# Performance work log

Hardware: AMD Instinct MI355X
Metric: run time of the kernel (lower is better)

Reference implementation:

```python
import jax, jax.numpy as jnp
import numpy as np

L1, L2, L3, L4 = 0.01, 0.001, 0.1, 100.0
DROP_P = 0.3

def setup_inputs() -> dict:
    key = jax.random.key(0)
    ks = jax.random.split(key, 6)
    n, p, h, c = 262144, 256, 256, 10
    x = jax.random.normal(ks[0], (n, p), dtype=jnp.float32)
    y = jax.random.randint(ks[1], (n,), 0, c, dtype=jnp.int64)
    drop_u = jax.random.uniform(ks[2], (n, h), dtype=jnp.float32)
    b1 = jax.random.normal(ks[3], (p, h), dtype=jnp.float32) / p
    b2 = jax.random.normal(ks[4], (h, c), dtype=jnp.float32) / h
    w = jax.random.normal(ks[5], (n, 1), dtype=jnp.float32) / n + 1.0 / np.sqrt(n).astype(np.float32)
    return {"x": x, "y": y, "drop_u": drop_u, "b1": b1, "b2": b2, "w": w}

def reference(x, y, drop_u, b1, b2, w):
    n, p = x.shape
    # MLP: ReLU -> Dropout(0.3) (inverted dropout, deterministic mask from drop_u)
    hdn = jax.nn.relu(x @ b1)
    keep = (drop_u > DROP_P).astype(x.dtype) / (1.0 - DROP_P)
    logits = (hdn * keep) @ b2  # [n, 10]
    pred = jnp.argmax(logits, axis=1)
    weight = w * w  # [n, 1]
    # per-sample CE; torch broadcast ce[n] * weight[n,1] -> [n,n], summed == ce.sum()*weight.sum()
    ce = -jnp.take_along_axis(jax.nn.log_softmax(logits, axis=-1), y[:, None], axis=1)[:, 0]
    loss = ce.sum() * weight.sum()
    # balancing regularizer: x.T @ diag(weight) @ x computed as column-scale-then-GEMM
    col = x.T @ weight  # [p, 1]
    gram = x.T @ (weight * x)  # [p, p] == x.T @ diag(weight) @ x
    bm = (gram - col @ col.T) * (1.0 - jnp.eye(p, dtype=x.dtype))
    loss = loss + L1 * (jnp.abs(b1).sum() + jnp.abs(b2).sum())
    loss = loss + L2 * jnp.sum(bm * bm)
    loss = loss + L3 * jnp.sum(weight * weight)
    loss = loss + L4 * (weight.sum() - 1.0) ** 2
    acc = jnp.mean((pred == y).astype(jnp.float32))
    return (loss, acc)
```

## Files before the change

### kernel.cpp

```cpp
#include <hip/hip_runtime.h>
#include <hip/hip_bf16.h>
#include <math.h>

typedef __bf16 v8bf  __attribute__((ext_vector_type(8)));
typedef __bf16 v4bf  __attribute__((ext_vector_type(4)));
typedef float  v16f  __attribute__((ext_vector_type(16)));
typedef float  v4f   __attribute__((ext_vector_type(4)));
typedef float  f4v   __attribute__((ext_vector_type(4)));

#define OFF_COL   16
#define OFF_WT    512
#define OFF_SLOT  262656
#define B1T_BYTE  68159488
#define B2T_BYTE  68290560
#define ZERO_BYTES 1088

extern "C" __global__ __launch_bounds__(256) void prep_k(
    const float* __restrict__ w, const float* __restrict__ b1,
    const float* __restrict__ b2, float* __restrict__ wsf) {
  float* weight = wsf + OFF_WT;
  __bf16* b1T = (__bf16*)((char*)wsf + B1T_BYTE);
  __bf16* b2T = (__bf16*)((char*)wsf + B2T_BYTE);
  int gid = blockIdx.x * 256 + threadIdx.x;
  float wi = w[gid];
  float wt = wi * wi;
  weight[gid] = wt;
  float s1 = wt, s2 = wt * wt, a1 = 0.f, a2 = 0.f;
  if (gid < 65536) {
    int h = gid >> 8, p = gid & 255;
    float v = b1[p * 256 + h];
    b1T[gid] = (__bf16)v;
    a1 = fabsf(v);
  }
  if (gid < 4096) {
    int c = gid >> 8, h = gid & 255;
    float v = (c < 10) ? b2[h * 10 + c] : 0.f;
    b2T[gid] = (__bf16)v;
    a2 = fabsf(v);
  }
  #pragma unroll
  for (int off = 32; off > 0; off >>= 1) {
    s1 += __shfl_down(s1, off);
    s2 += __shfl_down(s2, off);
    a1 += __shfl_down(a1, off);
    a2 += __shfl_down(a2, off);
  }
  if ((threadIdx.x & 63) == 0) {
    atomicAdd(&wsf[1], s1);
    atomicAdd(&wsf[2], s2);
    if (blockIdx.x < 256) atomicAdd(&wsf[3], a1);
    if (blockIdx.x < 16)  atomicAdd(&wsf[4], a2);
  }
}

extern "C" __global__ __launch_bounds__(512, 2) void gram_k(
    const float* __restrict__ x, float* __restrict__ wsf) {
  const float* weight = wsf + OFF_WT;
  float* slot = wsf + OFF_SLOT + blockIdx.x * 65536;
  __shared__ __bf16 xT[2][256 * 72];
  __shared__ __bf16 wxT[2][256 * 72];
  __shared__ float  wS[1024];
  const int tid = threadIdx.x;
  const int wv = tid >> 6, L = tid & 63;
  const int l32 = L & 31, lh = L >> 5;
  const int mb = 64 * (wv >> 1), nb = 128 * (wv & 1);
  const int col = tid & 255, rh = tid >> 8;
  const int base = blockIdx.x * 1024;
  v16f acc[2][4] = {};
  float colAcc = 0.f;
  float xv[32];

  wS[tid] = weight[base + tid];
  wS[tid + 512] = weight[base + 512 + tid];

  #pragma unroll
  for (int j = 0; j < 32; j++)
    xv[j] = x[(base + 32 * rh + j) * 256 + col];
  __syncthreads();
  #pragma unroll
  for (int s = 0; s < 8; s++) {
    v4bf xa, wa;
    #pragma unroll
    for (int i = 0; i < 4; i++) {
      int kr = 32 * rh + 4 * s + i;
      float v = xv[4 * s + i];
      float wvv = wS[kr] * v;
      colAcc += wvv;
      xa[i] = (__bf16)v;
      wa[i] = (__bf16)wvv;
    }
    *(v4bf*)&xT[0][col * 72 + 32 * rh + 4 * s]  = xa;
    *(v4bf*)&wxT[0][col * 72 + 32 * rh + 4 * s] = wa;
  }
  __syncthreads();

  for (int ch = 0; ch < 16; ch++) {
    const int cur = ch & 1, nxt = cur ^ 1;
    if (ch < 15) {
      int k0 = base + 64 * (ch + 1);
      #pragma unroll
      for (int j = 0; j < 32; j++)
        xv[j] = x[(k0 + 32 * rh + j) * 256 + col];
    }
    #pragma unroll
    for (int ks = 0; ks < 64; ks += 16) {
      v8bf a0 = *(const v8bf*)&xT[cur][(mb + l32) * 72 + ks + 8 * lh];
      v8bf a1 = *(const v8bf*)&xT[cur][(mb + 32 + l32) * 72 + ks + 8 * lh];
      v8bf b[4];
      #pragma unroll
      for (int tn = 0; tn < 4; tn++)
        b[tn] = *(const v8bf*)&wxT[cur][(nb + 32 * tn + l32) * 72 + ks + 8 * lh];
      #pragma unroll
      for (int tn = 0; tn < 4; tn++) {
        acc[0][tn] = __builtin_amdgcn_mfma_f32_32x32x16_bf16(a0, b[tn], acc[0][tn], 0, 0, 0);
        acc[1][tn] = __builtin_amdgcn_mfma_f32_32x32x16_bf16(a1, b[tn], acc[1][tn], 0, 0, 0);
      }
    }
    if (ch < 15) {
      const int wb = 64 * (ch + 1);
      #pragma unroll
      for (int s = 0; s < 8; s++) {
        v4bf xa, wa;
        #pragma unroll
        for (int i = 0; i < 4; i++) {
          int kr = 32 * rh + 4 * s + i;
          float v = xv[4 * s + i];
          float wvv = wS[wb + kr] * v;
          colAcc += wvv;
          xa[i] = (__bf16)v;
          wa[i] = (__bf16)wvv;
        }
        *(v4bf*)&xT[nxt][col * 72 + 32 * rh + 4 * s]  = xa;
        *(v4bf*)&wxT[nxt][col * 72 + 32 * rh + 4 * s] = wa;
      }
      __syncthreads();
    }
  }

  #pragma unroll
  for (int tm = 0; tm < 2; tm++)
    #pragma unroll
    for (int tn = 0; tn < 4; tn++)
      #pragma unroll
      for (int r = 0; r < 16; r++) {
        int row = mb + 32 * tm + (r & 3) + 8 * (r >> 2) + 4 * lh;
        int cg = nb + 32 * tn + l32;
        slot[row * 256 + cg] = acc[tm][tn][r];
      }
  atomicAdd(&wsf[OFF_COL + col], colAcc);
}

extern "C" __global__ __launch_bounds__(256) void gfin_k(float* __restrict__ wsf) {
  __shared__ float partial[4][256];
  const int tid = threadIdx.x;
  const int sg = tid >> 6, l = tid & 63;
  const int row = blockIdx.x;
  const float* slot0 = wsf + OFF_SLOT;
  f4v s = {0.f, 0.f, 0.f, 0.f};
  #pragma unroll 4
  for (int sl = sg; sl < 256; sl += 4)
    s += ((const f4v*)(slot0 + sl * 65536 + row * 256))[l];
  *(f4v*)&partial[sg][4 * l] = s;
  __syncthreads();
  float cr = wsf[OFF_COL + row];
  float ct = wsf[OFF_COL + tid];
  float gv = partial[0][tid] + partial[1][tid] + partial[2][tid] + partial[3][tid];
  float d = gv - cr * ct;
  float bm = (tid != row) ? d * d : 0.f;
  #pragma unroll
  for (int off = 32; off > 0; off >>= 1) bm += __shfl_down(bm, off);
  if (l == 0) atomicAdd(&wsf[5], bm);
}

extern "C" __global__ __launch_bounds__(256, 4) void mlp_k(
    const float* __restrict__ x, const int* __restrict__ y,
    const float* __restrict__ du, float* __restrict__ wsf) {
  const __bf16* b1T = (const __bf16*)((const char*)wsf + B1T_BYTE);
  const __bf16* b2T = (const __bf16*)((const char*)wsf + B2T_BYTE);
  __shared__ union U {
    struct { __bf16 xs[64 * 40]; __bf16 b1s[256 * 40]; } m;
    struct { __bf16 hk[64 * 264]; float lg[64 * 16]; } l;
  } sm;
  const int tid = threadIdx.x;
  const int wv = tid >> 6, L = tid & 63;
  const int l32 = L & 31, lh = L >> 5;
  const int nb = 64 * wv;
  const int rowBase = blockIdx.x * 64;

  v16f acc[2][2] = {};

  for (int kc = 0; kc < 256; kc += 32) {
    __syncthreads();
    #pragma unroll
    for (int i = 0; i < 2; i++) {
      int f = tid + 256 * i;
      int r = f >> 3, c4 = f & 7;
      f4v v = ((const f4v*)x)[(rowBase + r) * 64 + (kc >> 2) + c4];
      v4bf o;
      o[0] = (__bf16)v[0]; o[1] = (__bf16)v[1]; o[2] = (__bf16)v[2]; o[3] = (__bf16)v[3];
      *(v4bf*)&sm.m.xs[r * 40 + 4 * c4] = o;
    }
    #pragma unroll
    for (int i = 0; i < 4; i++) {
      int f = tid + 256 * i;
      int nr = f >> 2, c = f & 3;
      *(v8bf*)&sm.m.b1s[nr * 40 + 8 * c] = *(const v8bf*)&b1T[nr * 256 + kc + 8 * c];
    }
    __syncthreads();
    #pragma unroll
    for (int ks = 0; ks < 32; ks += 16) {
      v8bf a0 = *(const v8bf*)&sm.m.xs[(l32) * 40 + ks + 8 * lh];
      v8bf a1 = *(const v8bf*)&sm.m.xs[(32 + l32) * 40 + ks + 8 * lh];
      v8bf b0 = *(const v8bf*)&sm.m.b1s[(nb + l32) * 40 + ks + 8 * lh];
      v8bf b1f = *(const v8bf*)&sm.m.b1s[(nb + 32 + l32) * 40 + ks + 8 * lh];
      acc[0][0] = __builtin_amdgcn_mfma_f32_32x32x16_bf16(a0, b0,  acc[0][0], 0, 0, 0);
      acc[0][1] = __builtin_amdgcn_mfma_f32_32x32x16_bf16(a0, b1f, acc[0][1], 0, 0, 0);
      acc[1][0] = __builtin_amdgcn_mfma_f32_32x32x16_bf16(a1, b0,  acc[1][0], 0, 0, 0);
      acc[1][1] = __builtin_amdgcn_mfma_f32_32x32x16_bf16(a1, b1f, acc[1][1], 0, 0, 0);
    }
  }
  #pragma unroll
  for (int tm = 0; tm < 2; tm++)
    #pragma unroll
    for (int tn = 0; tn < 2; tn++)
      #pragma unroll
      for (int r = 0; r < 16; r++) {
        int row = 32 * tm + (r & 3) + 8 * (r >> 2) + 4 * lh;
        int cg = nb + 32 * tn + l32;
        float u = du[(rowBase + row) * 256 + cg];
        float v = acc[tm][tn][r];
        v = fmaxf(v, 0.f);
        acc[tm][tn][r] = (u > 0.3f) ? v * (1.0f / 0.7f) : 0.f;
      }

  __syncthreads();
  #pragma unroll
  for (int tm = 0; tm < 2; tm++)
    #pragma unroll
    for (int tn = 0; tn < 2; tn++)
      #pragma unroll
      for (int r = 0; r < 16; r++) {
        int row = 32 * tm + (r & 3) + 8 * (r >> 2) + 4 * lh;
        int cg = nb + 32 * tn + l32;
        sm.l.hk[row * 264 + cg] = (__bf16)acc[tm][tn][r];
      }
  __syncthreads();
  v4f lacc = {};
  #pragma unroll
  for (int kk = 0; kk < 8; kk++) {
    v8bf a  = *(const v8bf*)&sm.l.hk[(16 * wv + (L & 15)) * 264 + 32 * kk + 8 * (L >> 4)];
    v8bf bb = *(const v8bf*)&b2T[(L & 15) * 256 + 32 * kk + 8 * (L >> 4)];
    lacc = __builtin_amdgcn_mfma_f32_16x16x32_bf16(a, bb, lacc, 0, 0, 0);
  }
  #pragma unroll
  for (int r = 0; r < 4; r++)
    sm.l.lg[(16 * wv + 4 * (L >> 4) + r) * 16 + (L & 15)] = lacc[r];
  __syncthreads();
  float ce = 0.f;
  int cor = 0;
  if (tid < 64) {
    const float* lr = &sm.l.lg[tid * 16];
    float mx = lr[0];
    int am = 0;
    #pragma unroll
    for (int c = 1; c < 10; c++)
      if (lr[c] > mx) { mx = lr[c]; am = c; }
    float s = 0.f;
    #pragma unroll
    for (int c = 0; c < 10; c++) s += expf(lr[c] - mx);
    int yt = y[rowBase + tid];
    ce = logf(s) + mx - lr[yt];
    cor = (am == yt) ? 1 : 0;
  }
  if (wv == 0) {
    #pragma unroll
    for (int off = 32; off > 0; off >>= 1) ce += __shfl_down(ce, off);
    unsigned long long bal = __ballot(cor != 0);
    if (L == 0) {
      atomicAdd(&wsf[0], ce);
      atomicAdd((int*)&wsf[8], (int)__popcll(bal));
    }
  }
}

extern "C" __global__ void fin2_k(const float* __restrict__ wsf, float* __restrict__ out) {
  if (threadIdx.x == 0) {
    float ce = wsf[0], wsum = wsf[1], w4 = wsf[2], ab1 = wsf[3], ab2 = wsf[4], bm = wsf[5];
    int cor = ((const int*)wsf)[8];
    float loss = ce * wsum
               + 0.01f * (ab1 + ab2)
               + 0.001f * bm
               + 0.1f * w4
               + 100.f * (wsum - 1.f) * (wsum - 1.f);
    out[0] = loss;
    out[1] = (float)cor * (1.0f / 262144.0f);
  }
}

extern "C" void kernel_launch(void* const* d_in, const int* in_sizes, int n_in,
                              void* d_out, int out_size, void* d_ws, size_t ws_size,
                              hipStream_t stream) {
  const float* x  = (const float*)d_in[0];
  const int*   y  = (const int*)d_in[1];
  const float* du = (const float*)d_in[2];
  const float* b1 = (const float*)d_in[3];
  const float* b2 = (const float*)d_in[4];
  const float* w  = (const float*)d_in[5];
  float* wsf = (float*)d_ws;

  hipMemsetAsync(d_ws, 0, ZERO_BYTES, stream);
  prep_k<<<1024, 256, 0, stream>>>(w, b1, b2, wsf);
  gram_k<<<256, 512, 0, stream>>>(x, wsf);
  gfin_k<<<256, 256, 0, stream>>>(wsf);
  mlp_k<<<4096, 256, 0, stream>>>(x, y, du, wsf);
  fin2_k<<<1, 64, 0, stream>>>(wsf, (float*)d_out);
}
```

Measured before the change: 769.2 us.

## Register-prefetch next K-chunk of x/b1 and early-load dropout mask in mlp_k

The GEMM main loop now loads the next 32-wide K chunk of x and b1T into registers while MFMAs run on the current chunk in shared memory, which overlaps global latency with compute. Half of the dropout uniforms are loaded into registers during the second-to-last chunk so their latency is hidden before the epilogue. The logits scratch row stride is padded from 16 to 17 floats to avoid LDS bank conflicts. In exchange it adds register pressure (prefetch vectors plus 32 floats of dropout values) under a launch-bounds occupancy target of 4.

```diff
diff --git a/kernel.cpp b/kernel.cpp
--- a/kernel.cpp
+++ b/kernel.cpp
@@ -179,7 +179,7 @@
   const __bf16* b2T = (const __bf16*)((const char*)wsf + B2T_BYTE);
   __shared__ union U {
     struct { __bf16 xs[64 * 40]; __bf16 b1s[256 * 40]; } m;
-    struct { __bf16 hk[64 * 264]; float lg[64 * 16]; } l;
+    struct { __bf16 hk[64 * 264]; float lg[64 * 17]; } l;
   } sm;
   const int tid = threadIdx.x;
   const int wv = tid >> 6, L = tid & 63;
@@ -187,31 +187,62 @@
   const int nb = 64 * wv;
   const int rowBase = blockIdx.x * 64;
 
+  const int xr = tid >> 3, xc = tid & 7;
+  const int bnr = tid >> 2, bc = tid & 3;
+
   v16f acc[2][2] = {};
-
-  for (int kc = 0; kc < 256; kc += 32) {
+  f4v  xp0, xp1;
+  v8bf bp0, bp1, bp2, bp3;
+  float dup[32];
+
+  {
+    const int kc = 0;
+    xp0 = ((const f4v*)x)[(rowBase + xr) * 64 + (kc >> 2) + xc];
+    xp1 = ((const f4v*)x)[(rowBase + 32 + xr) * 64 + (kc >> 2) + xc];
+    bp0 = *(const v8bf*)&b1T[(bnr      ) * 256 + kc + 8 * bc];
+    bp1 = *(const v8bf*)&b1T[(bnr +  64) * 256 + kc + 8 * bc];
+    bp2 = *(const v8bf*)&b1T[(bnr + 128) * 256 + kc + 8 * bc];
+    bp3 = *(const v8bf*)&b1T[(bnr + 192) * 256 + kc + 8 * bc];
+  }
+
+  #pragma unroll
+  for (int ch = 0; ch < 8; ch++) {
     __syncthreads();
-    #pragma unroll
-    for (int i = 0; i < 2; i++) {
-      int f = tid + 256 * i;
-      int r = f >> 3, c4 = f & 7;
-      f4v v = ((const f4v*)x)[(rowBase + r) * 64 + (kc >> 2) + c4];
+    {
       v4bf o;
-      o[0] = (__bf16)v[0]; o[1] = (__bf16)v[1]; o[2] = (__bf16)v[2]; o[3] = (__bf16)v[3];
-      *(v4bf*)&sm.m.xs[r * 40 + 4 * c4] = o;
-    }
-    #pragma unroll
-    for (int i = 0; i < 4; i++) {
-      int f = tid + 256 * i;
-      int nr = f >> 2, c = f & 3;
-      *(v8bf*)&sm.m.b1s[nr * 40 + 8 * c] = *(const v8bf*)&b1T[nr * 256 + kc + 8 * c];
+      o[0] = (__bf16)xp0[0]; o[1] = (__bf16)xp0[1]; o[2] = (__bf16)xp0[2]; o[3] = (__bf16)xp0[3];
+      *(v4bf*)&sm.m.xs[xr * 40 + 4 * xc] = o;
+      o[0] = (__bf16)xp1[0]; o[1] = (__bf16)xp1[1]; o[2] = (__bf16)xp1[2]; o[3] = (__bf16)xp1[3];
+      *(v4bf*)&sm.m.xs[(xr + 32) * 40 + 4 * xc] = o;
+      *(v8bf*)&sm.m.b1s[(bnr      ) * 40 + 8 * bc] = bp0;
+      *(v8bf*)&sm.m.b1s[(bnr +  64) * 40 + 8 * bc] = bp1;
+      *(v8bf*)&sm.m.b1s[(bnr + 128) * 40 + 8 * bc] = bp2;
+      *(v8bf*)&sm.m.b1s[(bnr + 192) * 40 + 8 * bc] = bp3;
     }
     __syncthreads();
+    if (ch < 7) {
+      const int kc = 32 * (ch + 1);
+      xp0 = ((const f4v*)x)[(rowBase + xr) * 64 + (kc >> 2) + xc];
+      xp1 = ((const f4v*)x)[(rowBase + 32 + xr) * 64 + (kc >> 2) + xc];
+      bp0 = *(const v8bf*)&b1T[(bnr      ) * 256 + kc + 8 * bc];
+      bp1 = *(const v8bf*)&b1T[(bnr +  64) * 256 + kc + 8 * bc];
+      bp2 = *(const v8bf*)&b1T[(bnr + 128) * 256 + kc + 8 * bc];
+      bp3 = *(const v8bf*)&b1T[(bnr + 192) * 256 + kc + 8 * bc];
+    }
+    if (ch == 6) {
+      #pragma unroll
+      for (int tn = 0; tn < 2; tn++)
+        #pragma unroll
+        for (int r = 0; r < 16; r++) {
+          int row = (r & 3) + 8 * (r >> 2) + 4 * lh;
+          dup[tn * 16 + r] = du[(rowBase + row) * 256 + nb + 32 * tn + l32];
+        }
+    }
     #pragma unroll
     for (int ks = 0; ks < 32; ks += 16) {
-      v8bf a0 = *(const v8bf*)&sm.m.xs[(l32) * 40 + ks + 8 * lh];
-      v8bf a1 = *(const v8bf*)&sm.m.xs[(32 + l32) * 40 + ks + 8 * lh];
-      v8bf b0 = *(const v8bf*)&sm.m.b1s[(nb + l32) * 40 + ks + 8 * lh];
+      v8bf a0  = *(const v8bf*)&sm.m.xs[(l32) * 40 + ks + 8 * lh];
+      v8bf a1  = *(const v8bf*)&sm.m.xs[(32 + l32) * 40 + ks + 8 * lh];
+      v8bf b0  = *(const v8bf*)&sm.m.b1s[(nb + l32) * 40 + ks + 8 * lh];
       v8bf b1f = *(const v8bf*)&sm.m.b1s[(nb + 32 + l32) * 40 + ks + 8 * lh];
       acc[0][0] = __builtin_amdgcn_mfma_f32_32x32x16_bf16(a0, b0,  acc[0][0], 0, 0, 0);
       acc[0][1] = __builtin_amdgcn_mfma_f32_32x32x16_bf16(a0, b1f, acc[0][1], 0, 0, 0);
@@ -220,18 +251,22 @@
     }
   }
   #pragma unroll
-  for (int tm = 0; tm < 2; tm++)
-    #pragma unroll
-    for (int tn = 0; tn < 2; tn++)
-      #pragma unroll
-      for (int r = 0; r < 16; r++) {
-        int row = 32 * tm + (r & 3) + 8 * (r >> 2) + 4 * lh;
-        int cg = nb + 32 * tn + l32;
-        float u = du[(rowBase + row) * 256 + cg];
-        float v = acc[tm][tn][r];
-        v = fmaxf(v, 0.f);
-        acc[tm][tn][r] = (u > 0.3f) ? v * (1.0f / 0.7f) : 0.f;
-      }
+  for (int tn = 0; tn < 2; tn++)
+    #pragma unroll
+    for (int r = 0; r < 16; r++) {
+      float u = dup[tn * 16 + r];
+      float v = fmaxf(acc[0][tn][r], 0.f);
+      acc[0][tn][r] = (u > 0.3f) ? v * (1.0f / 0.7f) : 0.f;
+    }
+  #pragma unroll
+  for (int tn = 0; tn < 2; tn++)
+    #pragma unroll
+    for (int r = 0; r < 16; r++) {
+      int row = 32 + (r & 3) + 8 * (r >> 2) + 4 * lh;
+      float u = du[(rowBase + row) * 256 + nb + 32 * tn + l32];
+      float v = fmaxf(acc[1][tn][r], 0.f);
+      acc[1][tn][r] = (u > 0.3f) ? v * (1.0f / 0.7f) : 0.f;
+    }
 
   __syncthreads();
   #pragma unroll
@@ -254,12 +289,12 @@
   }
   #pragma unroll
   for (int r = 0; r < 4; r++)
-    sm.l.lg[(16 * wv + 4 * (L >> 4) + r) * 16 + (L & 15)] = lacc[r];
+    sm.l.lg[(16 * wv + 4 * (L >> 4) + r) * 17 + (L & 15)] = lacc[r];
   __syncthreads();
   float ce = 0.f;
   int cor = 0;
   if (tid < 64) {
-    const float* lr = &sm.l.lg[tid * 16];
+    const float* lr = &sm.l.lg[tid * 17];
     float mx = lr[0];
     int am = 0;
     #pragma unroll
```

Result: slower. 807.8 us (+5.0%).

## Prefetch dropout uniforms during GEMM loop and pack into shared bitmask

Applied to the files above, without the earlier changes.

The dropout uniforms used to be read with scattered scalar global loads after the first GEMM. They are now streamed as coalesced float4 loads spread across the k-chunk loop, using a small register ring that hides load latency behind the MFMA work. Each load is converted into a 4-bit keep mask in shared memory, and the epilogue reads that mask instead of global memory. The logits staging array is also padded to stride 17 to cut LDS bank conflicts. In exchange the kernel holds 24 more live float registers, which could reduce occupancy at 4 waves per SIMD, and it uses 4 KB more LDS in the GEMM phase.

```diff
diff --git a/kernel.cpp b/kernel.cpp
--- a/kernel.cpp
+++ b/kernel.cpp
@@ -178,18 +178,22 @@
   const __bf16* b1T = (const __bf16*)((const char*)wsf + B1T_BYTE);
   const __bf16* b2T = (const __bf16*)((const char*)wsf + B2T_BYTE);
   __shared__ union U {
-    struct { __bf16 xs[64 * 40]; __bf16 b1s[256 * 40]; } m;
-    struct { __bf16 hk[64 * 264]; float lg[64 * 16]; } l;
+    struct { __bf16 xs[64 * 40]; __bf16 b1s[256 * 40]; unsigned char msk[4096]; } m;
+    struct { __bf16 hk[64 * 264]; float lg[64 * 17]; } l;
   } sm;
   const int tid = threadIdx.x;
   const int wv = tid >> 6, L = tid & 63;
   const int l32 = L & 31, lh = L >> 5;
   const int nb = 64 * wv;
   const int rowBase = blockIdx.x * 64;
+  const f4v* du4 = (const f4v*)du + (size_t)rowBase * 64;
 
   v16f acc[2][2] = {};
-
-  for (int kc = 0; kc < 256; kc += 32) {
+  f4v dq[6];
+
+  #pragma unroll
+  for (int ch = 0; ch < 8; ch++) {
+    const int kc = 32 * ch;
     __syncthreads();
     #pragma unroll
     for (int i = 0; i < 2; i++) {
@@ -207,11 +211,24 @@
       *(v8bf*)&sm.m.b1s[nr * 40 + 8 * c] = *(const v8bf*)&b1T[nr * 256 + kc + 8 * c];
     }
     __syncthreads();
+    dq[(2 * ch) % 6]     = du4[tid + 256 * (2 * ch)];
+    dq[(2 * ch + 1) % 6] = du4[tid + 256 * (2 * ch + 1)];
+    if (ch >= 2) {
+      const int i0 = 2 * ch - 4, i1 = 2 * ch - 3;
+      f4v d0 = dq[i0 % 6];
+      sm.m.msk[tid + 256 * i0] = (unsigned char)(
+          (d0[0] > 0.3f ? 1 : 0) | (d0[1] > 0.3f ? 2 : 0) |
+          (d0[2] > 0.3f ? 4 : 0) | (d0[3] > 0.3f ? 8 : 0));
+      f4v d1 = dq[i1 % 6];
+      sm.m.msk[tid + 256 * i1] = (unsigned char)(
+          (d1[0] > 0.3f ? 1 : 0) | (d1[1] > 0.3f ? 2 : 0) |
+          (d1[2] > 0.3f ? 4 : 0) | (d1[3] > 0.3f ? 8 : 0));
+    }
     #pragma unroll
     for (int ks = 0; ks < 32; ks += 16) {
-      v8bf a0 = *(const v8bf*)&sm.m.xs[(l32) * 40 + ks + 8 * lh];
-      v8bf a1 = *(const v8bf*)&sm.m.xs[(32 + l32) * 40 + ks + 8 * lh];
-      v8bf b0 = *(const v8bf*)&sm.m.b1s[(nb + l32) * 40 + ks + 8 * lh];
+      v8bf a0  = *(const v8bf*)&sm.m.xs[(l32) * 40 + ks + 8 * lh];
+      v8bf a1  = *(const v8bf*)&sm.m.xs[(32 + l32) * 40 + ks + 8 * lh];
+      v8bf b0  = *(const v8bf*)&sm.m.b1s[(nb + l32) * 40 + ks + 8 * lh];
       v8bf b1f = *(const v8bf*)&sm.m.b1s[(nb + 32 + l32) * 40 + ks + 8 * lh];
       acc[0][0] = __builtin_amdgcn_mfma_f32_32x32x16_bf16(a0, b0,  acc[0][0], 0, 0, 0);
       acc[0][1] = __builtin_amdgcn_mfma_f32_32x32x16_bf16(a0, b1f, acc[0][1], 0, 0, 0);
@@ -220,6 +237,15 @@
     }
   }
   #pragma unroll
+  for (int i = 12; i < 16; i++) {
+    f4v d = dq[i % 6];
+    sm.m.msk[tid + 256 * i] = (unsigned char)(
+        (d[0] > 0.3f ? 1 : 0) | (d[1] > 0.3f ? 2 : 0) |
+        (d[2] > 0.3f ? 4 : 0) | (d[3] > 0.3f ? 8 : 0));
+  }
+  __syncthreads();
+
+  #pragma unroll
   for (int tm = 0; tm < 2; tm++)
     #pragma unroll
     for (int tn = 0; tn < 2; tn++)
@@ -227,10 +253,9 @@
       for (int r = 0; r < 16; r++) {
         int row = 32 * tm + (r & 3) + 8 * (r >> 2) + 4 * lh;
         int cg = nb + 32 * tn + l32;
-        float u = du[(rowBase + row) * 256 + cg];
-        float v = acc[tm][tn][r];
-        v = fmaxf(v, 0.f);
-        acc[tm][tn][r] = (u > 0.3f) ? v * (1.0f / 0.7f) : 0.f;
+        unsigned char mb2 = sm.m.msk[row * 64 + (cg >> 2)];
+        float v = fmaxf(acc[tm][tn][r], 0.f);
+        acc[tm][tn][r] = ((mb2 >> (l32 & 3)) & 1) ? v * (1.0f / 0.7f) : 0.f;
       }
 
   __syncthreads();
@@ -254,12 +279,12 @@
   }
   #pragma unroll
   for (int r = 0; r < 4; r++)
-    sm.l.lg[(16 * wv + 4 * (L >> 4) + r) * 16 + (L & 15)] = lacc[r];
+    sm.l.lg[(16 * wv + 4 * (L >> 4) + r) * 17 + (L & 15)] = lacc[r];
   __syncthreads();
   float ce = 0.f;
   int cor = 0;
   if (tid < 64) {
-    const float* lr = &sm.l.lg[tid * 16];
+    const float* lr = &sm.l.lg[tid * 17];
     float mx = lr[0];
     int am = 0;
     #pragma unroll
```

Result: slower. 863.7 us (+12.3%).
